# Kernel tuning notes

Hardware: AMD Instinct MI355X
Metric: run time of the kernel (lower is better)

The kernel has to match this reference:

```python
import jax, jax.numpy as jnp
import numpy as np
from jax import lax

D_MODEL = 200
N_LAYER = 12
NHEADS = 8
HEADDIM = 50
D_STATE = 64
D_INNER = 2 * D_MODEL            # 400
CONV_DIM = D_INNER + 2 * D_STATE  # 528 (ngroups=1)
D_IN_PROJ = 2 * D_INNER + 2 * D_STATE + NHEADS  # 936
D_CONV = 4
EPS = 1e-5


def rmsnorm(x, w):
    v = jnp.mean(jnp.square(x), axis=-1, keepdims=True)
    return x * lax.rsqrt(v + EPS) * w


def groupnorm(x, groups, g, b):
    B, C, H, W = x.shape
    xg = x.reshape(B, groups, C // groups, H, W)
    mu = jnp.mean(xg, axis=(2, 3, 4), keepdims=True)
    var = jnp.mean(jnp.square(xg - mu), axis=(2, 3, 4), keepdims=True)
    xn = ((xg - mu) * lax.rsqrt(var + EPS)).reshape(B, C, H, W)
    return xn * g[:, None, None] + b[:, None, None]


def patch_embed(x, pe_conv_w, proj_in_w, gn_g, gn_b, spec_w):
    b, c, l, d = x.shape
    # time path: 'b c l d' -> (b, 1, c*l, d), conv -> (b, 25, c*l, 8)
    time_x = x.reshape(b, 1, c * l, d)
    t = lax.conv_general_dilated(time_x, proj_in_w, (1, 25), ((0, 0), (24, 24)),
                                 dimension_numbers=('NCHW', 'OIHW', 'NCHW'))
    t = jax.nn.gelu(groupnorm(t, 5, gn_g, gn_b), approximate=False)
    time_emb = t.transpose(0, 2, 1, 3).reshape(b, c, l, D_MODEL)
    # freq path: rfft over patch dim, norm='forward'
    spec = jnp.abs(jnp.fft.rfft(x, axis=-1, norm='forward'))  # (b,c,l,101)
    spec_emb = jnp.einsum('bclf,df->bcld', spec, spec_w)
    patch = time_emb + spec_emb
    # depthwise 7x7 positional conv over (d, c, l)
    pos = lax.conv_general_dilated(patch.transpose(0, 3, 1, 2), pe_conv_w, (1, 1),
                                   ((3, 3), (3, 3)),
                                   dimension_numbers=('NCHW', 'OIHW', 'NCHW'),
                                   feature_group_count=D_MODEL)
    return patch + pos.transpose(0, 2, 3, 1)


def ssd_scan(xh, dt, B, C, A, D):
    # xh: (b,l,h,p)  dt: (b,l,h)  B,C: (b,l,n)  A,D: (h,)
    b, l, h, p = xh.shape

    def step(state, inp):
        x_t, dt_t, B_t, C_t = inp
        dA = jnp.exp(dt_t * A)  # (b,h)
        state = state * dA[:, :, None, None] + \
            (dt_t[:, :, None, None] * x_t[:, :, :, None]) * B_t[:, None, None, :]
        y = jnp.einsum('bhpn,bn->bhp', state, C_t)
        return state, y

    state0 = jnp.zeros((b, h, p, D_STATE), xh.dtype)
    _, ys = lax.scan(step, state0,
                     (xh.transpose(1, 0, 2, 3), dt.transpose(1, 0, 2),
                      B.transpose(1, 0, 2), C.transpose(1, 0, 2)))
    return ys.transpose(1, 0, 2, 3) + xh * D[None, None, :, None]


def mamba2(u, in_w, conv_w, conv_b, dt_bias, A_log, D, gn_w, out_w):
    b, l, _ = u.shape
    zxbcdt = u @ in_w.T  # (b,l,936)
    z = zxbcdt[..., :D_INNER]
    xBC = zxbcdt[..., D_INNER:D_INNER + CONV_DIM]
    dt = jax.nn.softplus(zxbcdt[..., D_INNER + CONV_DIM:] + dt_bias)  # (b,l,8)
    # causal depthwise conv1d, kernel 4
    xc = lax.conv_general_dilated(xBC.transpose(0, 2, 1), conv_w, (1,), ((D_CONV - 1, 0),),
                                  dimension_numbers=('NCH', 'OIH', 'NCH'),
                                  feature_group_count=CONV_DIM)
    xBC = jax.nn.silu((xc + conv_b[:, None]).transpose(0, 2, 1))
    x = xBC[..., :D_INNER].reshape(b, l, NHEADS, HEADDIM)
    Bm = xBC[..., D_INNER:D_INNER + D_STATE]
    Cm = xBC[..., D_INNER + D_STATE:]
    y = ssd_scan(x, dt, Bm, Cm, -jnp.exp(A_log), D).reshape(b, l, D_INNER)
    y = rmsnorm(y * jax.nn.silu(z), gn_w)  # RMSNormGated, norm_before_gate=False
    return y @ out_w.T


@jax.checkpoint
def layer(hidden, residual, norm_w, in_w, conv_w, conv_b, dt_bias, A_log, D, gn_w, out_w):
    residual = hidden + residual
    hidden = mamba2(rmsnorm(residual, norm_w), in_w, conv_w, conv_b, dt_bias, A_log, D, gn_w, out_w)
    return hidden, residual


def forward(x, pe_conv_w, proj_in_w, gn_g, gn_b, spec_w, norm_w, in_proj_w, conv_w, conv_b,
            dt_bias, A_log, D, gnorm_w, out_proj_w, norm_f_w, head_w, head_b):
    b, c, l, d = x.shape
    hidden = patch_embed(x, pe_conv_w, proj_in_w, gn_g, gn_b, spec_w).reshape(b, c * l, d)
    residual = jnp.zeros_like(hidden)
    for i in range(N_LAYER):
        hidden, residual = layer(hidden, residual, norm_w[i], in_proj_w[i], conv_w[i],
                                 conv_b[i], dt_bias[i], A_log[i], D[i], gnorm_w[i], out_proj_w[i])
    hidden = rmsnorm(hidden + residual, norm_f_w).reshape(b, c, l, d)
    return hidden @ head_w.T + head_b


def setup_inputs():
    key = jax.random.key(0)
    ks = jax.random.split(key, 12)
    B, CH, L, P = 16, 19, 30, 200

    def g(k, shape, scale):
        return jax.random.normal(k, shape, jnp.float32) * scale

    dt = jax.random.uniform(ks[8], (N_LAYER, NHEADS), jnp.float32, 1e-3, 0.1)
    return {
        'x': g(ks[0], (B, CH, L, P), 1.0),
        'pe_conv_w': g(ks[1], (D_MODEL, 1, 7, 7), 0.15),
        'proj_in_w': g(ks[2], (25, 1, 1, 49), 0.14),
        'gn_g': jnp.ones(25, jnp.float32),
        'gn_b': jnp.zeros(25, jnp.float32),
        'spec_w': g(ks[3], (D_MODEL, 101), 0.1),
        'norm_w': jnp.ones((N_LAYER, D_MODEL), jnp.float32),
        'in_proj_w': g(ks[4], (N_LAYER, D_IN_PROJ, D_MODEL), 0.07),
        'conv_w': g(ks[5], (N_LAYER, CONV_DIM, 1, D_CONV), 0.4),
        'conv_b': jnp.zeros((N_LAYER, CONV_DIM), jnp.float32),
        'dt_bias': jnp.log(jnp.expm1(dt)),
        'A_log': jnp.log(jax.random.uniform(ks[9], (N_LAYER, NHEADS), jnp.float32, 1.0, 16.0)),
        'D': jnp.ones((N_LAYER, NHEADS), jnp.float32),
        'gnorm_w': jnp.ones((N_LAYER, D_INNER), jnp.float32),
        'out_proj_w': g(ks[6], (N_LAYER, D_MODEL, D_INNER), 0.05),
        'norm_f_w': jnp.ones(D_MODEL, jnp.float32),
        'head_w': g(ks[7], (D_MODEL, D_MODEL), 0.07),
        'head_b': jnp.zeros(D_MODEL, jnp.float32),
    }


def reference(x, pe_conv_w, proj_in_w, gn_g, gn_b, spec_w, norm_w, in_proj_w, conv_w, conv_b,
              dt_bias, A_log, D, gnorm_w, out_proj_w, norm_f_w, head_w, head_b):
    return forward(x, pe_conv_w, proj_in_w, gn_g, gn_b, spec_w, norm_w, in_proj_w, conv_w,
                   conv_b, dt_bias, A_log, D, gnorm_w, out_proj_w, norm_f_w, head_w, head_b)
```

## Files before the change

kernel.cpp:

```cpp
#include <hip/hip_runtime.h>
#include <hip/hip_bf16.h>
#include <math.h>

#define D_MODEL   200
#define N_LAYER   12
#define NHEADS    8
#define HEADDIM   50
#define D_STATE   64
#define D_INNER   400
#define CONV_DIM  528
#define D_IN_PROJ 936
#define D_CONV    4
#define EPS       1e-5f

#define BATCH 16
#define CH    19
#define LLEN  30
#define SEQ   570
#define NTOK  9120
#define NFREQ 101

typedef __attribute__((ext_vector_type(8))) short s8v;
typedef __attribute__((ext_vector_type(4))) float f32x4;

__device__ __forceinline__ short f2bf(float f) {
    unsigned u = __float_as_uint(f);
    u += 0x7FFFu + ((u >> 16) & 1u);
    return (short)(u >> 16);
}

__global__ __launch_bounds__(256) void gemm_bf16(
    const short* __restrict__ A, const short* __restrict__ W,
    const float* __restrict__ bias, float* __restrict__ C,
    int M, int N, int Kp, int accum)
{
    __shared__ __align__(16) short As[128][40];
    __shared__ __align__(16) short Ws[128][40];

    int bm = blockIdx.y * 128;
    int bn = blockIdx.x * 128;
    int tid = threadIdx.x;
    int lane = tid & 63;
    int wv = tid >> 6;
    int wm = wv & 1, wn = wv >> 1;
    int lm = lane & 15, lg = lane >> 4;

    int sr = tid >> 1;
    int sh_ = (tid & 1) * 16;

    f32x4 acc[4][4];
#pragma unroll
    for (int i = 0; i < 4; i++)
#pragma unroll
        for (int j = 0; j < 4; j++) acc[i][j] = (f32x4)0.f;

    for (int k0 = 0; k0 < Kp; k0 += 32) {
        {
            s8v v0 = (s8v)0, v1 = (s8v)0;
            if (bm + sr < M) {
                const short* ga = A + (size_t)(bm + sr) * Kp + k0 + sh_;
                v0 = *(const s8v*)ga;
                v1 = *(const s8v*)(ga + 8);
            }
            *(s8v*)&As[sr][sh_] = v0;
            *(s8v*)&As[sr][sh_ + 8] = v1;
        }
        {
            s8v v0 = (s8v)0, v1 = (s8v)0;
            if (bn + sr < N) {
                const short* gw = W + (size_t)(bn + sr) * Kp + k0 + sh_;
                v0 = *(const s8v*)gw;
                v1 = *(const s8v*)(gw + 8);
            }
            *(s8v*)&Ws[sr][sh_] = v0;
            *(s8v*)&Ws[sr][sh_ + 8] = v1;
        }
        __syncthreads();

        s8v af[4], bf[4];
#pragma unroll
        for (int i = 0; i < 4; i++)
            af[i] = *(const s8v*)&As[wm * 64 + i * 16 + lm][lg * 8];
#pragma unroll
        for (int j = 0; j < 4; j++)
            bf[j] = *(const s8v*)&Ws[wn * 64 + j * 16 + lm][lg * 8];
#pragma unroll
        for (int i = 0; i < 4; i++)
#pragma unroll
            for (int j = 0; j < 4; j++)
                acc[i][j] = __builtin_amdgcn_mfma_f32_16x16x32_bf16(
                    af[i], bf[j], acc[i][j], 0, 0, 0);
        __syncthreads();
    }

#pragma unroll
    for (int j = 0; j < 4; j++) {
        int n = bn + wn * 64 + j * 16 + lm;
        if (n >= N) continue;
        float bv = bias ? bias[n] : 0.f;
#pragma unroll
        for (int i = 0; i < 4; i++) {
            int mbase = bm + wm * 64 + i * 16 + lg * 4;
#pragma unroll
            for (int r = 0; r < 4; r++) {
                int m = mbase + r;
                if (m >= M) continue;
                size_t idx = (size_t)m * N + n;
                float v = acc[i][j][r] + bv;
                if (accum) v += C[idx];
                C[idx] = v;
            }
        }
    }
}

__global__ __launch_bounds__(256) void gemm_nt(
    const float* __restrict__ A, const float* __restrict__ W,
    const float* __restrict__ bias, float* __restrict__ C,
    int M, int N, int K, int accum)
{
    const int BM = 128, BK = 16;
    __shared__ float As[16][BM + 4];
    __shared__ float Ws[16][BM + 4];

    int bm = blockIdx.y * BM;
    int bn = blockIdx.x * BM;
    int tid = threadIdx.x;
    int lr = tid >> 1;
    int lc = (tid & 1) * 8;
    int tx = tid & 15;
    int ty = tid >> 4;

    float acc[8][8];
#pragma unroll
    for (int i = 0; i < 8; i++)
#pragma unroll
        for (int j = 0; j < 8; j++) acc[i][j] = 0.f;

    for (int k0 = 0; k0 < K; k0 += BK) {
#pragma unroll
        for (int i = 0; i < 8; i++) {
            int gr = bm + lr, gk = k0 + lc + i;
            As[lc + i][lr] = (gr < M && gk < K) ? A[(size_t)gr * K + gk] : 0.f;
        }
#pragma unroll
        for (int i = 0; i < 8; i++) {
            int gr = bn + lr, gk = k0 + lc + i;
            Ws[lc + i][lr] = (gr < N && gk < K) ? W[(size_t)gr * K + gk] : 0.f;
        }
        __syncthreads();
#pragma unroll
        for (int kk = 0; kk < BK; kk++) {
            float a[8], bv[8];
#pragma unroll
            for (int i = 0; i < 8; i++) a[i] = As[kk][ty * 8 + i];
#pragma unroll
            for (int j = 0; j < 8; j++) bv[j] = Ws[kk][tx * 8 + j];
#pragma unroll
            for (int i = 0; i < 8; i++)
#pragma unroll
                for (int j = 0; j < 8; j++)
                    acc[i][j] = fmaf(a[i], bv[j], acc[i][j]);
        }
        __syncthreads();
    }

#pragma unroll
    for (int i = 0; i < 8; i++) {
        int gm = bm + ty * 8 + i;
        if (gm >= M) continue;
#pragma unroll
        for (int j = 0; j < 8; j++) {
            int gn = bn + tx * 8 + j;
            if (gn >= N) continue;
            float v = acc[i][j];
            if (bias) v += bias[gn];
            if (accum) v += C[(size_t)gm * N + gn];
            C[(size_t)gm * N + gn] = v;
        }
    }
}

// ... 158 lines not shown
#pragma unroll
    for (int k = 0; k < 49; k++) wreg[k] = wl[k * 16 + dd];

    for (int o = tid; o < 4 * 30 * 16; o += 256) {
        int r2 = o >> 4;
        int l = r2 % 30, ci = r2 / 30;
        int c = c0 + ci;
        if (c >= CH) continue;
        float acc = pl[((ci + 3) * 30 + l) * 16 + dd];
#pragma unroll
        for (int i = 0; i < 7; i++) {
#pragma unroll
            for (int j = 0; j < 7; j++) {
                int ll = l + j - 3;
                if (ll < 0 || ll >= LLEN) continue;
                acc = fmaf(pl[((ci + i) * 30 + ll) * 16 + dd], wreg[i * 7 + j], acc);
            }
        }
        if (d < 200) hidden[((size_t)(b * CH + c) * LLEN + l) * 200 + d] = acc;
    }
}

__global__ __launch_bounds__(64) void add_rmsnorm_kernel(
    const float* __restrict__ hidden, float* __restrict__ residual,
    const float* __restrict__ wn, float* __restrict__ u,
    short* __restrict__ ubf, int first)
{
    int m = blockIdx.x;
    int lane = threadIdx.x;
    const float* hr = hidden + (size_t)m * 200;
    float* rr = residual + (size_t)m * 200;
    float v[4];
    float ss = 0.f;
#pragma unroll
    for (int i = 0; i < 4; i++) {
        int k = lane + i * 64;
        float xv = 0.f;
        if (k < 200) {
            xv = hr[k] + (first ? 0.f : rr[k]);
            rr[k] = xv;
        }
        v[i] = xv;
        ss = fmaf(xv, xv, ss);
    }
#pragma unroll
    for (int o = 32; o; o >>= 1) ss += __shfl_xor(ss, o, 64);
    float rstd = rsqrtf(ss * (1.f / 200.f) + EPS);
#pragma unroll
    for (int i = 0; i < 4; i++) {
        int k = lane + i * 64;
        float val = v[i] * rstd * ((k < 200) ? wn[k] : 0.f);
        if (k < 200 && u) u[(size_t)m * 200 + k] = val;
        if (ubf) {
            if (k < 200) ubf[(size_t)m * 224 + k] = f2bf(val);
            else if (k < 224) ubf[(size_t)m * 224 + k] = 0;
        }
    }
}

__global__ __launch_bounds__(256) void norm_dt_kernel(
    const float* __restrict__ hidden, float* __restrict__ residual,
    const float* __restrict__ wn, short* __restrict__ ubf,
    const float* __restrict__ Win, const float* __restrict__ dt_bias,
    float* __restrict__ dtb, int layer, int first)
{
    int m = blockIdx.x;
    int tid = threadIdx.x;
    __shared__ float su[200];
    __shared__ float rs[4];
    float xv = 0.f;
    if (tid < 200) {
        xv = hidden[(size_t)m * 200 + tid] + (first ? 0.f : residual[(size_t)m * 200 + tid]);
        residual[(size_t)m * 200 + tid] = xv;
    }
    float ss = xv * xv;
#pragma unroll
    for (int o = 32; o; o >>= 1) ss += __shfl_xor(ss, o, 64);
    int lane = tid & 63, w = tid >> 6;
    if (lane == 0) rs[w] = ss;
    __syncthreads();
    float rstd = rsqrtf((rs[0] + rs[1] + rs[2] + rs[3]) * (1.f / 200.f) + EPS);
    if (tid < 200) {
        float val = xv * rstd * wn[tid];
        su[tid] = val;
        ubf[(size_t)m * 224 + tid] = f2bf(val);
    } else if (tid < 224) {
        ubf[(size_t)m * 224 + tid] = 0;
    }
    __syncthreads();
    int h = tid >> 5, l = tid & 31;
    const float* wr = Win + (size_t)layer * D_IN_PROJ * 200 + (size_t)(928 + h) * 200;
    float s = 0.f;
    for (int k = l; k < 200; k += 32) s = fmaf(su[k], wr[k], s);
    s += __shfl_xor(s, 16, 32);
    s += __shfl_xor(s, 8, 32);
    s += __shfl_xor(s, 4, 32);
    s += __shfl_xor(s, 2, 32);
    s += __shfl_xor(s, 1, 32);
    if (l == 0) {
        float raw = s + dt_bias[layer * NHEADS + h];
        dtb[(size_t)m * NHEADS + h] = (raw > 20.f) ? raw : log1pf(expf(raw));
    }
}

__global__ __launch_bounds__(256) void dt_gemv_kernel(
    const float* __restrict__ u, const float* __restrict__ Win,
    const float* __restrict__ dt_bias, float* __restrict__ dtb, int layer)
{
    int tid = threadIdx.x;
    int tok = blockIdx.x * 4 + (tid >> 6);
    int head = (tid >> 3) & 7;
    int l8 = tid & 7;
    const float* ur = u + (size_t)tok * 200;
    const float* wr = Win + (size_t)layer * D_IN_PROJ * 200 + (size_t)(928 + head) * 200;
    float s = 0.f;
    for (int k = l8; k < 200; k += 8) s = fmaf(ur[k], wr[k], s);
    s += __shfl_xor(s, 1, 64);
    s += __shfl_xor(s, 2, 64);
    s += __shfl_xor(s, 4, 64);
    if (l8 == 0) {
        float raw = s + dt_bias[layer * NHEADS + head];
        dtb[(size_t)tok * NHEADS + head] = (raw > 20.f) ? raw : log1pf(expf(raw));
    }
}

__global__ __launch_bounds__(256) void dtconv2_kernel(
    const float* __restrict__ zxbcdt, const float* __restrict__ cw,
    const float* __restrict__ cb, float* __restrict__ xBC, int layer)
{
    int b = blockIdx.x, tt = blockIdx.y;
    int t0 = tt * 8;
    __shared__ float zs[11][528];
    const float* cwl = cw + (size_t)layer * CONV_DIM * 4;
    const float* cbl = cb + (size_t)layer * CONV_DIM;
    for (int i = threadIdx.x; i < 11 * 528; i += 256) {
        int r = i / 528, ch = i - r * 528;
        int t = t0 - 3 + r;
        zs[r][ch] = (t >= 0 && t < SEQ)
                        ? zxbcdt[(size_t)(b * SEQ + t) * D_IN_PROJ + D_INNER + ch] : 0.f;
    }
    __syncthreads();
    for (int o = threadIdx.x; o < 8 * 528; o += 256) {
        int tr = o / 528, ch = o - tr * 528;
        int t = t0 + tr;
        if (t >= SEQ) continue;
        float acc = cbl[ch];
#pragma unroll
        for (int k = 0; k < 4; k++)
            acc = fmaf(zs[tr + k][ch], cwl[ch * 4 + k], acc);
        xBC[(size_t)(b * SEQ + t) * CONV_DIM + ch] = acc / (1.f + expf(-acc));
    }
}

__global__ __launch_bounds__(512) void ssd_scanA_kernel(
    const float* __restrict__ xBC, const float* __restrict__ dtb,
    const float* __restrict__ A_log, const float* __restrict__ Dv,
    float* __restrict__ ylocal, float* __restrict__ Pref,
    float* __restrict__ Sbuf, float* __restrict__ Pd,
    int layer, int lchunk, int nchunk)
{
    int b = blockIdx.x, c = blockIdx.y;
    int tid = threadIdx.x;
    int h = tid >> 6, p = tid & 63;
    float A = -expf(A_log[layer * NHEADS + h]);
    float Dh = Dv[layer * NHEADS + h];

    __shared__ __align__(16) float sh[3][2][536];
    int t0 = c * lchunk;
    int npairs = lchunk >> 1;

    for (int j = 0; j < 2 && j < npairs; j++) {
        if (tid < 264) {
            int wch = (tid >= 132) ? 1 : 0;
            int fidx = tid - wch * 132;
            int tq = t0 + 2 * j + wch;
            float4 v = ((const float4*)(xBC + (size_t)(b * SEQ + tq) * CONV_DIM))[fidx];
            *(float4*)&sh[j][wch][fidx * 4] = v;
        } else if (tid < 280) {
            int e = tid - 264, tok = e >> 3, hd = e & 7;
            sh[j][tok][528 + hd] = dtb[(size_t)(b * SEQ + t0 + 2 * j + tok) * NHEADS + hd];
        }
    }
    __syncthreads();

    float s[64];
#pragma unroll
    for (int n = 0; n < 64; n++) s[n] = 0.f;
    float pacc = 1.f;

    for (int i = 0; i < npairs; i++) {
        int t = t0 + 2 * i;
        int buf = i % 3;
        int nb = (i + 2) % 3;
        bool pf = (i + 2 < npairs);
        float4 rx;
        float rdt = 0.f;
        int wch = 0, fidx = 0;
        if (pf) {
            if (tid < 264) {
                wch = (tid >= 132) ? 1 : 0;
                fidx = tid - wch * 132;
                int tq = t + 4 + wch;
                rx = ((const float4*)(xBC + (size_t)(b * SEQ + tq) * CONV_DIM))[fidx];
            } else if (tid < 280) {
                int e = tid - 264, tok = e >> 3, hd = e & 7;
                rdt = dtb[(size_t)(b * SEQ + t + 4 + tok) * NHEADS + hd];
            }
        }
#pragma unroll
        for (int k = 0; k < 2; k++) {
            float dtv = sh[buf][k][528 + h];
            float xp  = (p < HEADDIM) ? sh[buf][k][h * HEADDIM + p] : 0.f;
            float dA = __expf(dtv * A);
            float u  = dtv * xp;
            pacc *= dA;
            const float4* B4 = (const float4*)&sh[buf][k][D_INNER];
            const float4* C4 = (const float4*)&sh[buf][k][D_INNER + D_STATE];
            float y0 = 0.f, y1 = 0.f, y2 = 0.f, y3 = 0.f;
#pragma unroll
            for (int n4 = 0; n4 < 16; n4++) {
                float4 bq = B4[n4];
                float4 cq = C4[n4];
                float t0v = fmaf(s[4 * n4 + 0], dA, u * bq.x);
                float t1v = fmaf(s[4 * n4 + 1], dA, u * bq.y);
                float t2v = fmaf(s[4 * n4 + 2], dA, u * bq.z);
                float t3v = fmaf(s[4 * n4 + 3], dA, u * bq.w);
                s[4 * n4 + 0] = t0v; s[4 * n4 + 1] = t1v;
                s[4 * n4 + 2] = t2v; s[4 * n4 + 3] = t3v;
                y0 = fmaf(t0v, cq.x, y0);
                y1 = fmaf(t1v, cq.y, y1);
                y2 = fmaf(t2v, cq.z, y2);
                y3 = fmaf(t3v, cq.w, y3);
            }
            if (p < HEADDIM)
                ylocal[(size_t)(b * SEQ + t + k) * D_INNER + h * HEADDIM + p] =
                    fmaf(xp, Dh, (y0 + y1) + (y2 + y3));
            if (p == 0)
                Pref[(size_t)(b * SEQ + t + k) * NHEADS + h] = pacc;
        }
        if (pf) {
            if (tid < 264) *(float4*)&sh[nb][wch][fidx * 4] = rx;
            else if (tid < 280) { int e = tid - 264; sh[nb][e >> 3][528 + (e & 7)] = rdt; }
        }
        __syncthreads();
    }

    if (p < HEADDIM) {
        float* Sb = Sbuf + ((size_t)((b * NHEADS + h) * nchunk + c)) * (HEADDIM * 64)
                    + p * 64;
#pragma unroll
        for (int n4 = 0; n4 < 16; n4++)
            ((float4*)Sb)[n4] = make_float4(s[4 * n4], s[4 * n4 + 1],
                                            s[4 * n4 + 2], s[4 * n4 + 3]);
    }
    if (p == 0) Pd[(b * NHEADS + h) * nchunk + c] = pacc;
}

__global__ __launch_bounds__(512) void ssd_state_kernel(
    const float* __restrict__ xBC, const float* __restrict__ dtb,
    const float* __restrict__ A_log, float* __restrict__ Sbuf,
    float* __restrict__ Pd, int layer, int lchunk, int nchunk)
{
    int b = blockIdx.x, c = blockIdx.y;
    int tid = threadIdx.x;
    int h = tid >> 6, p = tid & 63;
    float A = -expf(A_log[layer * NHEADS + h]);

    __shared__ float sh[2][544];
    int t0 = c * lchunk, tend = t0 + lchunk;

    {
        const float* base = xBC + (size_t)(b * SEQ + t0) * CONV_DIM;
        sh[0][tid] = base[tid];
        if (tid < 24) {
            int e2 = 512 + tid;
            sh[0][e2] = (e2 < 528) ? base[e2]
                                   : dtb[(size_t)(b * SEQ + t0) * NHEADS + (e2 - 528)];
        }
    }
    __syncthreads();

    float s[64];
#pragma unroll
    for (int n = 0; n < 64; n++) s[n] = 0.f;
    float pacc = 1.f;

    for (int t = t0; t < tend; t++) {
        int cur = (t - t0) & 1, nxt = cur ^ 1;
        float pf0 = 0.f, pf1 = 0.f;
        if (t + 1 < tend) {
            const float* base = xBC + (size_t)(b * SEQ + t + 1) * CONV_DIM;
            pf0 = base[tid];
            if (tid < 24) {
                int e2 = 512 + tid;
                pf1 = (e2 < 528) ? base[e2]
                                 : dtb[(size_t)(b * SEQ + t + 1) * NHEADS + (e2 - 528)];
            }
        }
        float dtv = sh[cur][528 + h];
        float xp  = (p < HEADDIM) ? sh[cur][h * HEADDIM + p] : 0.f;
        float dA = __expf(dtv * A);
        float u  = dtv * xp;
        pacc *= dA;
        const float4* B4 = (const float4*)&sh[cur][D_INNER];
#pragma unroll
        for (int n4 = 0; n4 < 16; n4++) {
            float4 bq = B4[n4];
            s[4 * n4 + 0] = fmaf(s[4 * n4 + 0], dA, u * bq.x);
            s[4 * n4 + 1] = fmaf(s[4 * n4 + 1], dA, u * bq.y);
            s[4 * n4 + 2] = fmaf(s[4 * n4 + 2], dA, u * bq.z);
            s[4 * n4 + 3] = fmaf(s[4 * n4 + 3], dA, u * bq.w);
        }
        if (t + 1 < tend) {
            sh[nxt][tid] = pf0;
            if (tid < 24) sh[nxt][512 + tid] = pf1;
        }
        __syncthreads();
    }

    if (p < HEADDIM) {
        float* Sb = Sbuf + ((size_t)((b * NHEADS + h) * nchunk + c)) * (HEADDIM * 64)
                    + p * 64;
#pragma unroll
        for (int n4 = 0; n4 < 16; n4++)
            ((float4*)Sb)[n4] = make_float4(s[4 * n4], s[4 * n4 + 1],
                                            s[4 * n4 + 2], s[4 * n4 + 3]);
    }
    if (p == 0) Pd[(b * NHEADS + h) * nchunk + c] = pacc;
}

__global__ __launch_bounds__(256) void ssd_scan2b_kernel(
    float* __restrict__ Sbuf, const float* __restrict__ Pd, int nchunk)
{
    int bh = blockIdx.x;
    int e = blockIdx.y * 256 + threadIdx.x;
    if (e >= HEADDIM * 64) return;
    float* base = Sbuf + (size_t)bh * nchunk * (HEADDIM * 64) + e;
    const float* pd = Pd + bh * nchunk;
    float cur = 0.f;
    for (int c = 0; c < nchunk; c++) {
        float l = base[(size_t)c * (HEADDIM * 64)];
        base[(size_t)c * (HEADDIM * 64)] = cur;
        cur = fmaf(pd[c], cur, l);
    }
}

__global__ __launch_bounds__(512) void ssd_corr_kernel(
    const float* __restrict__ xBC, const float* __restrict__ zxbcdt,
    const float* __restrict__ ylocal, const float* __restrict__ Pref,
    const float* __restrict__ Sbuf, const float* __restrict__ gw,
    short* __restrict__ ybf, int layer, int lchunk, int nchunk)
{
    int b = blockIdx.x, c = blockIdx.y;
    int tid = threadIdx.x;
    int h = tid >> 6, p = tid & 63;
    float gval = (p < HEADDIM) ? gw[(size_t)layer * D_INNER + h * HEADDIM + p] : 0.f;

    __shared__ __align__(16) float Cst[2][2][64];
    __shared__ float pfs[2][2][8];
    __shared__ float red[2][2][8];
    int t0 = c * lchunk;
    int npairs = lchunk >> 1;

    float s0[64];
    if (p < HEADDIM) {
        const float* Sb = Sbuf + ((size_t)((b * NHEADS + h) * nchunk + c)) * (HEADDIM * 64)
                          + p * 64;
#pragma unroll
        for (int n4 = 0; n4 < 16; n4++) {
            float4 v = ((const float4*)Sb)[n4];
            s0[4 * n4] = v.x; s0[4 * n4 + 1] = v.y;
            s0[4 * n4 + 2] = v.z; s0[4 * n4 + 3] = v.w;
        }
    } else {
#pragma unroll
        for (int n = 0; n < 64; n++) s0[n] = 0.f;
    }

    int col = h * HEADDIM + ((p < HEADDIM) ? p : 0);

    if (tid < 128) {
        int k = tid >> 6, n = tid & 63;
        Cst[0][k][n] = xBC[(size_t)(b * SEQ + t0 + k) * CONV_DIM + D_INNER + D_STATE + n];
    } else if (tid < 144) {
        int e = tid - 128, k = e >> 3, hd = e & 7;
        pfs[0][k][hd] = Pref[(size_t)(b * SEQ + t0 + k) * NHEADS + hd];
    }
    float ylr[2], zvr[2];
#pragma unroll
    for (int k = 0; k < 2; k++) {
        ylr[k] = ylocal[(size_t)(b * SEQ + t0 + k) * D_INNER + col];
        zvr[k] = zxbcdt[(size_t)(b * SEQ + t0 + k) * D_IN_PROJ + col];
    }
    __syncthreads();

    for (int i = 0; i < npairs; i++) {
        int t = t0 + 2 * i;
        int buf = i & 1, nb = buf ^ 1;
        bool pf = (i + 1 < npairs);
        float rc = 0.f, rpf = 0.f, yln[2], zvn[2];
        if (pf) {
            if (tid < 128) {
                int k = tid >> 6, n = tid & 63;
                rc = xBC[(size_t)(b * SEQ + t + 2 + k) * CONV_DIM + D_INNER + D_STATE + n];
            } else if (tid < 144) {
                int e = tid - 128, k = e >> 3, hd = e & 7;
                rpf = Pref[(size_t)(b * SEQ + t + 2 + k) * NHEADS + hd];
            }
#pragma unroll
            for (int k = 0; k < 2; k++) {
                yln[k] = ylocal[(size_t)(b * SEQ + t + 2 + k) * D_INNER + col];
                zvn[k] = zxbcdt[(size_t)(b * SEQ + t + 2 + k) * D_IN_PROJ + col];
            }
        }
        float g0 = 0.f, g1 = 0.f;
#pragma unroll
        for (int k = 0; k < 2; k++) {
            const float4* C4 = (const float4*)&Cst[buf][k][0];
            float c0 = 0.f, c1 = 0.f, c2 = 0.f, c3 = 0.f;
#pragma unroll
            for (int n4 = 0; n4 < 16; n4++) {
                float4 cq = C4[n4];
                c0 = fmaf(s0[4 * n4 + 0], cq.x, c0);
                c1 = fmaf(s0[4 * n4 + 1], cq.y, c1);
                c2 = fmaf(s0[4 * n4 + 2], cq.z, c2);
                c3 = fmaf(s0[4 * n4 + 3], cq.w, c3);
            }
            float corr = (c0 + c1) + (c2 + c3);
            float yv = fmaf(pfs[buf][k][h], corr, ylr[k]);
            float zv = zvr[k];
            float gg = yv * (zv / (1.f + expf(-zv)));
            gg = (p < HEADDIM) ? gg : 0.f;
            if (k == 0) g0 = gg; else g1 = gg;
        }
        float gs0 = g0 * g0, gs1 = g1 * g1;
#pragma unroll
        for (int o = 32; o; o >>= 1) {
            gs0 += __shfl_xor(gs0, o, 64);
            gs1 += __shfl_xor(gs1, o, 64);
        }
        if (p == 0) { red[buf][0][h] = gs0; red[buf][1][h] = gs1; }
        if (pf) {
            if (tid < 128) { int k = tid >> 6, n = tid & 63; Cst[nb][k][n] = rc; }
            else if (tid < 144) { int e = tid - 128; pfs[nb][e >> 3][e & 7] = rpf; }
            ylr[0] = yln[0]; ylr[1] = yln[1];
            zvr[0] = zvn[0]; zvr[1] = zvn[1];
        }
        __syncthreads();
        float tot0 = (red[buf][0][0] + red[buf][0][1]) + (red[buf][0][2] + red[buf][0][3]) +
                     (red[buf][0][4] + red[buf][0][5]) + (red[buf][0][6] + red[buf][0][7]);
        float tot1 = (red[buf][1][0] + red[buf][1][1]) + (red[buf][1][2] + red[buf][1][3]) +
                     (red[buf][1][4] + red[buf][1][5]) + (red[buf][1][6] + red[buf][1][7]);
        float rstd0 = rsqrtf(tot0 * (1.f / D_INNER) + EPS);
        float rstd1 = rsqrtf(tot1 * (1.f / D_INNER) + EPS);
        size_t row0 = (size_t)(b * SEQ + t) * 416;
        size_t row1 = (size_t)(b * SEQ + t + 1) * 416;
        if (p < HEADDIM) {
            ybf[row0 + h * HEADDIM + p] = f2bf(g0 * rstd0 * gval);
            ybf[row1 + h * HEADDIM + p] = f2bf(g1 * rstd1 * gval);
        } else {
            int widx = h * 14 + (p - HEADDIM);
            if (widx < 16) {
                ybf[row0 + 400 + widx] = 0;
                ybf[row1 + 400 + widx] = 0;
            }
        }
    }
}

__global__ __launch_bounds__(512) void ssd_out_kernel(
    const float* __restrict__ xBC, const float* __restrict__ dtb,
    const float* __restrict__ A_log, const float* __restrict__ Dv,
    const float* __restrict__ Sbuf, float* __restrict__ y,
    int layer, int lchunk, int nchunk)
{
    int b = blockIdx.x, c = blockIdx.y;
    int tid = threadIdx.x;
    int h = tid >> 6, p = tid & 63;
    float A = -expf(A_log[layer * NHEADS + h]);
    float Dh = Dv[layer * NHEADS + h];

    __shared__ float sh[2][544];
    int t0 = c * lchunk, tend = t0 + lchunk;

    {
        const float* base = xBC + (size_t)(b * SEQ + t0) * CONV_DIM;
        sh[0][tid] = base[tid];
        if (tid < 24) {
            int e2 = 512 + tid;
            sh[0][e2] = (e2 < 528) ? base[e2]
                                   : dtb[(size_t)(b * SEQ + t0) * NHEADS + (e2 - 528)];
        }
    }

    float s[64];
    if (p < HEADDIM) {
        const float* Sb = Sbuf + ((size_t)((b * NHEADS + h) * nchunk + c)) * (HEADDIM * 64)
                          + p * 64;
#pragma unroll
        for (int n4 = 0; n4 < 16; n4++) {
            float4 v = ((const float4*)Sb)[n4];
            s[4 * n4] = v.x; s[4 * n4 + 1] = v.y; s[4 * n4 + 2] = v.z; s[4 * n4 + 3] = v.w;
        }
    } else {
#pragma unroll
        for (int n = 0; n < 64; n++) s[n] = 0.f;
    }
    __syncthreads();

    for (int t = t0; t < tend; t++) {
        int cur = (t - t0) & 1, nxt = cur ^ 1;
        float pf0 = 0.f, pf1 = 0.f;
        if (t + 1 < tend) {
            const float* base = xBC + (size_t)(b * SEQ + t + 1) * CONV_DIM;
            pf0 = base[tid];
            if (tid < 24) {
                int e2 = 512 + tid;
                pf1 = (e2 < 528) ? base[e2]
                                 : dtb[(size_t)(b * SEQ + t + 1) * NHEADS + (e2 - 528)];
            }
        }
        float dtv = sh[cur][528 + h];
        float xp  = (p < HEADDIM) ? sh[cur][h * HEADDIM + p] : 0.f;
        float dA = __expf(dtv * A);
        float u  = dtv * xp;
        const float4* B4 = (const float4*)&sh[cur][D_INNER];
        const float4* C4 = (const float4*)&sh[cur][D_INNER + D_STATE];
        float y0 = 0.f, y1 = 0.f, y2 = 0.f, y3 = 0.f;
#pragma unroll
        for (int n4 = 0; n4 < 16; n4++) {
            float4 bq = B4[n4];
            float4 cq = C4[n4];
            float t0v = fmaf(s[4 * n4 + 0], dA, u * bq.x);
            float t1v = fmaf(s[4 * n4 + 1], dA, u * bq.y);
            float t2v = fmaf(s[4 * n4 + 2], dA, u * bq.z);
            float t3v = fmaf(s[4 * n4 + 3], dA, u * bq.w);
            s[4 * n4 + 0] = t0v; s[4 * n4 + 1] = t1v;
            s[4 * n4 + 2] = t2v; s[4 * n4 + 3] = t3v;
            y0 = fmaf(t0v, cq.x, y0);
            y1 = fmaf(t1v, cq.y, y1);
            y2 = fmaf(t2v, cq.z, y2);
            y3 = fmaf(t3v, cq.w, y3);
        }
        if (p < HEADDIM) {
            float yv = (y0 + y1) + (y2 + y3);
            y[(size_t)(b * SEQ + t) * D_INNER + h * HEADDIM + p] = fmaf(xp, Dh, yv);
        }
        if (t + 1 < tend) {
            sh[nxt][tid] = pf0;
            if (tid < 24) sh[nxt][512 + tid] = pf1;
        }
        __syncthreads();
    }
}

__global__ __launch_bounds__(256) void gate_norm_kernel(
    float* __restrict__ y, const float* __restrict__ zxbcdt,
    const float* __restrict__ gw, short* __restrict__ ybf, int layer)
{
    int m = blockIdx.x;
    __shared__ float buf[D_INNER];
    __shared__ float red[4];
    const float* z = zxbcdt + (size_t)m * D_IN_PROJ;
    float* yr = y + (size_t)m * D_INNER;
    const float* gwl = gw + (size_t)layer * D_INNER;
    float ss = 0.f;
    for (int k = threadIdx.x; k < D_INNER; k += 256) {
        float zv = z[k];
        float sz = zv / (1.f + expf(-zv));
        float g = yr[k] * sz;
        buf[k] = g;
        ss = fmaf(g, g, ss);
    }
    int lane = threadIdx.x & 63, w = threadIdx.x >> 6;
#pragma unroll
    for (int o = 32; o; o >>= 1) ss += __shfl_xor(ss, o, 64);
    if (lane == 0) red[w] = ss;
    __syncthreads();
    float tot = red[0] + red[1] + red[2] + red[3];
    float rstd = rsqrtf(tot * (1.f / D_INNER) + EPS);
    for (int k = threadIdx.x; k < 416; k += 256) {
        if (k < D_INNER) {
            float v = buf[k] * rstd * gwl[k];
            yr[k] = v;
            if (ybf) ybf[(size_t)m * 416 + k] = f2bf(v);
        } else if (ybf) {
            ybf[(size_t)m * 416 + k] = 0;
        }
    }
}

extern "C" void kernel_launch(void* const* d_in, const int* in_sizes, int n_in,
                              void* d_out, int out_size, void* d_ws, size_t ws_size,
                              hipStream_t stream)
{
    const float* x         = (const float*)d_in[0];
    const float* pe_conv_w = (const float*)d_in[1];
    const float* proj_in_w = (const float*)d_in[2];
    const float* gn_g      = (const float*)d_in[3];
    const float* gn_b      = (const float*)d_in[4];
    const float* spec_w    = (const float*)d_in[5];
    const float* norm_w    = (const float*)d_in[6];
    const float* in_proj_w = (const float*)d_in[7];
    const float* conv_w    = (const float*)d_in[8];
    const float* conv_b    = (const float*)d_in[9];
    const float* dt_bias   = (const float*)d_in[10];
    const float* A_log     = (const float*)d_in[11];
    const float* Dv        = (const float*)d_in[12];
    const float* gnorm_w   = (const float*)d_in[13];
    const float* out_proj_w= (const float*)d_in[14];
    const float* norm_f_w  = (const float*)d_in[15];
    const float* head_w    = (const float*)d_in[16];
    const float* head_b    = (const float*)d_in[17];
    float* out = (float*)d_out;
    float* ws  = (float*)d_ws;

    const size_t needA = 31650304ull * sizeof(float);
    int fast = (ws_size >= needA) ? 1 : 0;

    int nchunk, lchunk;
    float *residual = ws, *hidden = ws + 1824000;
    float *zxbcdt, *xBC, *dtb, *Sbuf, *Pd;
    float *ubuf = nullptr, *ybuf = nullptr, *ybuf_s = nullptr, *Pref = nullptr;
    short *w_in_bf = nullptr, *w_out_bf = nullptr, *w_head_bf = nullptr,
          *w_spec_bf = nullptr, *csmat_bf = nullptr, *x_bf = nullptr,
          *ubuf_bf = nullptr, *ybuf_bf = nullptr, *magb_bf = nullptr;

    if (fast) {
        nchunk = 15; lchunk = 38;
        zxbcdt = ws + 3648000;
        xBC    = ws + 12184320;
        dtb    = ws + 16999680;
        Sbuf   = ws + 17072640;
        Pd     = ws + 23216640;
        short* pool = (short*)(ws + 23218560);
        w_in_bf   = pool;
        w_out_bf  = pool + 2515968;
        w_head_bf = pool + 3514368;
        w_spec_bf = pool + 3559168;
        ubuf_bf   = pool + 3584768;
        ybuf_bf   = pool + 5627648;
        ybuf_s    = ws + 27929344;
        Pref      = ws + 31577344;
        csmat_bf  = (short*)(Sbuf + 4000000);
        x_bf      = (short*)(Sbuf + 4100000);
        magb_bf   = (short*)(Sbuf + 5200000);
    } else {
        nchunk = 6; lchunk = 95;
        ubuf   = ws + 3648000;
        zxbcdt = ws + 5472000;
        xBC    = ws + 14008320;
        dtb    = ws + 18823680;
        ybuf   = ws + 18896640;
        Sbuf   = ws + 1824000;
        Pd     = ws + 5470000;
    }

    float* traw  = fast ? Sbuf : ybuf;
    float* patch = zxbcdt;
    float* csout = fast ? (Sbuf + 2000000) : (xBC + 50000);
    float* csmat = xBC;
    float* magb  = fast ? nullptr : (xBC + 2000000);
    float* stats = dtb;

    if (fast) {
        cast_pad_kernel<<<(12 * 936 * 224 + 255) / 256, 256, 0, stream>>>(
            in_proj_w, w_in_bf, 12 * 936, 200, 224);
        cast_pad_kernel<<<(12 * 200 * 416 + 255) / 256, 256, 0, stream>>>(
            out_proj_w, w_out_bf, 12 * 200, 400, 416);
        cast_pad_kernel<<<(200 * 224 + 255) / 256, 256, 0, stream>>>(
            head_w, w_head_bf, 200, 200, 224);
        cast_pad_kernel<<<(200 * 128 + 255) / 256, 256, 0, stream>>>(
            spec_w, w_spec_bf, 200, 101, 128);
        cast_pad_kernel<<<(9120 * 224 + 255) / 256, 256, 0, stream>>>(
            x, x_bf, 9120, 200, 224);
        dft_init_bf_kernel<<<(202 * 224 + 255) / 256, 256, 0, stream>>>(csmat_bf);
    } else {
        dft_init_kernel<<<(202 * 200 + 255) / 256, 256, 0, stream>>>(csmat);
    }

    time_conv_kernel<<<NTOK, 256, 0, stream>>>(x, proj_in_w, traw);
    gn_stats_kernel<<<80, 256, 0, stream>>>(traw, stats);
    gn_gelu_kernel<<<(NTOK * 200 + 255) / 256, 256, 0, stream>>>(traw, stats, gn_g, gn_b, patch);
    if (fast) {
        gemm_bf16<<<dim3(2, 72), 256, 0, stream>>>(x_bf, csmat_bf, nullptr, csout,
                                                   NTOK, 202, 224, 0);
        mag_bf_kernel<<<(NTOK * 128 + 255) / 256, 256, 0, stream>>>(csout, magb_bf);
        gemm_bf16<<<dim3(2, 72), 256, 0, stream>>>(magb_bf, w_spec_bf, nullptr, patch,
                                                   NTOK, 200, 128, 1);
    } else {
        gemm_nt<<<dim3(2, 72), 256, 0, stream>>>(x, csmat, nullptr, csout, NTOK, 202, 200, 0);
        mag_kernel<<<(NTOK * NFREQ + 255) / 256, 256, 0, stream>>>(csout, magb);
        gemm_nt<<<dim3(2, 72), 256, 0, stream>>>(magb, spec_w, nullptr, patch,
                                                 NTOK, 200, NFREQ, 1);
    }
    pe_conv3_kernel<<<dim3(16, 13, 5), 256, 0, stream>>>(patch, pe_conv_w, hidden);

    for (int i = 0; i < N_LAYER; i++) {
        if (fast) {
            norm_dt_kernel<<<NTOK, 256, 0, stream>>>(hidden, residual, norm_w + i * 200,
                                                     ubuf_bf, in_proj_w, dt_bias, dtb,
                                                     i, (i == 0) ? 1 : 0);
            gemm_bf16<<<dim3(8, 72), 256, 0, stream>>>(
                ubuf_bf, w_in_bf + (size_t)i * 936 * 224, nullptr, zxbcdt,
                NTOK, D_IN_PROJ, 224, 0);
        } else {
            add_rmsnorm_kernel<<<NTOK, 64, 0, stream>>>(hidden, residual, norm_w + i * 200,
                                                        ubuf, nullptr, (i == 0) ? 1 : 0);
            dt_gemv_kernel<<<NTOK / 4, 256, 0, stream>>>(ubuf, in_proj_w, dt_bias, dtb, i);
            gemm_nt<<<dim3(8, 72), 256, 0, stream>>>(
                ubuf, in_proj_w + (size_t)i * D_IN_PROJ * 200, nullptr, zxbcdt,
                NTOK, D_IN_PROJ, 200, 0);
        }
        dtconv2_kernel<<<dim3(16, 72), 256, 0, stream>>>(zxbcdt, conv_w, conv_b, xBC, i);
        {
            dim3 g(BATCH, nchunk);
            if (fast) {
                ssd_scanA_kernel<<<g, 512, 0, stream>>>(xBC, dtb, A_log, Dv,
                                                        ybuf_s, Pref, Sbuf, Pd,
                                                        i, lchunk, nchunk);
                ssd_scan2b_kernel<<<dim3(BATCH * NHEADS, 13), 256, 0, stream>>>(Sbuf, Pd, nchunk);
                ssd_corr_kernel<<<g, 512, 0, stream>>>(
                    xBC, zxbcdt, ybuf_s, Pref, Sbuf, gnorm_w, ybuf_bf, i, lchunk, nchunk);
                gemm_bf16<<<dim3(2, 72), 256, 0, stream>>>(
                    ybuf_bf, w_out_bf + (size_t)i * 200 * 416, nullptr, hidden,
                    NTOK, 200, 416, 0);
            } else {
                ssd_state_kernel<<<g, 512, 0, stream>>>(xBC, dtb, A_log, Sbuf, Pd,
                                                        i, lchunk, nchunk);
                ssd_scan2b_kernel<<<dim3(BATCH * NHEADS, 13), 256, 0, stream>>>(Sbuf, Pd, nchunk);
                ssd_out_kernel<<<g, 512, 0, stream>>>(xBC, dtb, A_log, Dv, Sbuf, ybuf,
                                                      i, lchunk, nchunk);
                gate_norm_kernel<<<NTOK, 256, 0, stream>>>(ybuf, zxbcdt, gnorm_w, nullptr, i);
                gemm_nt<<<dim3(2, 72), 256, 0, stream>>>(
                    ybuf, out_proj_w + (size_t)i * 200 * D_INNER, nullptr, hidden,
                    NTOK, 200, D_INNER, 0);
            }
        }
    }

    add_rmsnorm_kernel<<<NTOK, 64, 0, stream>>>(hidden, residual, norm_f_w,
                                                fast ? nullptr : ubuf,
                                                fast ? ubuf_bf : nullptr, 0);
    if (fast) {
        gemm_bf16<<<dim3(2, 72), 256, 0, stream>>>(ubuf_bf, w_head_bf, head_b, out,
                                                   NTOK, 200, 224, 0);
    } else {
        gemm_nt<<<dim3(2, 72), 256, 0, stream>>>(ubuf, head_w, head_b, out,
                                                 NTOK, 200, 200, 0);
    }
}
```

Baseline: 2.565 ms.

## Restructure chunked SSD scan into state-only pass plus fused output rescan with bf16 B/C

Replaces the scanA pass, which produced local outputs, prefix decays and chunk states, and the correction pass with two kernels. The first pass now computes only the chunk-final states. The second pass rescans each chunk from the carried-in state, computing the output, gate and norm directly. This drops the ylocal and Pref intermediate buffers and their global traffic, and shrinks the workspace. It costs recomputing the recurrence twice. B and C are staged in shared memory as bf16, which lowers LDS footprint and bandwidth but loses precision in the state update.

```diff
diff --git a/kernel.cpp b/kernel.cpp
--- a/kernel.cpp
+++ b/kernel.cpp
@@ -28,6 +28,13 @@
     u += 0x7FFFu + ((u >> 16) & 1u);
     return (short)(u >> 16);
 }
+__device__ __forceinline__ uint2 packbf4(float4 v) {
+    unsigned a = (unsigned short)f2bf(v.x), b = (unsigned short)f2bf(v.y);
+    unsigned c = (unsigned short)f2bf(v.z), d = (unsigned short)f2bf(v.w);
+    return make_uint2(a | (b << 16), c | (d << 16));
+}
+__device__ __forceinline__ float bflo(unsigned d) { return __uint_as_float(d << 16); }
+__device__ __forceinline__ float bfhi(unsigned d) { return __uint_as_float(d & 0xffff0000u); }
 
 __global__ __launch_bounds__(256) void gemm_bf16(
     const short* __restrict__ A, const short* __restrict__ W,
@@ -492,33 +499,35 @@
     }
 }
 
-__global__ __launch_bounds__(512) void ssd_scanA_kernel(
+__global__ __launch_bounds__(512) void ssd_state4_kernel(
     const float* __restrict__ xBC, const float* __restrict__ dtb,
-    const float* __restrict__ A_log, const float* __restrict__ Dv,
-    float* __restrict__ ylocal, float* __restrict__ Pref,
-    float* __restrict__ Sbuf, float* __restrict__ Pd,
-    int layer, int lchunk, int nchunk)
+    const float* __restrict__ A_log, float* __restrict__ Sbuf,
+    float* __restrict__ Pd, int layer, int lchunk, int nchunk)
 {
     int b = blockIdx.x, c = blockIdx.y;
     int tid = threadIdx.x;
     int h = tid >> 6, p = tid & 63;
     float A = -expf(A_log[layer * NHEADS + h]);
-    float Dh = Dv[layer * NHEADS + h];
-
-    __shared__ __align__(16) float sh[3][2][536];
+
+    __shared__ __align__(16) float shx[2][2][400];
+    __shared__ __align__(16) uint2 shB[2][2][16];
+    __shared__ float shdt[2][2][8];
     int t0 = c * lchunk;
     int npairs = lchunk >> 1;
 
-    for (int j = 0; j < 2 && j < npairs; j++) {
-        if (tid < 264) {
-            int wch = (tid >= 132) ? 1 : 0;
-            int fidx = tid - wch * 132;
-            int tq = t0 + 2 * j + wch;
-            float4 v = ((const float4*)(xBC + (size_t)(b * SEQ + tq) * CONV_DIM))[fidx];
-            *(float4*)&sh[j][wch][fidx * 4] = v;
-        } else if (tid < 280) {
-            int e = tid - 264, tok = e >> 3, hd = e & 7;
-            sh[j][tok][528 + hd] = dtb[(size_t)(b * SEQ + t0 + 2 * j + tok) * NHEADS + hd];
+    {
+        if (tid < 200) {
+            int tok = (tid >= 100) ? 1 : 0;
+            int fidx = tid - tok * 100;
+            float4 v = ((const float4*)(xBC + (size_t)(b * SEQ + t0 + tok) * CONV_DIM))[fidx];
+            *(float4*)&shx[0][tok][fidx * 4] = v;
+        } else if (tid < 232) {
+            int e = tid - 200, tok = e >> 4, q = e & 15;
+            float4 v = ((const float4*)(xBC + (size_t)(b * SEQ + t0 + tok) * CONV_DIM))[100 + q];
+            shB[0][tok][q] = packbf4(v);
+        } else if (tid < 248) {
+            int e = tid - 232, tok = e >> 3, hd = e & 7;
+            shdt[0][tok][hd] = dtb[(size_t)(b * SEQ + t0 + tok) * NHEADS + hd];
         }
     }
     __syncthreads();
@@ -530,57 +539,52 @@
 
     for (int i = 0; i < npairs; i++) {
         int t = t0 + 2 * i;
-        int buf = i % 3;
-        int nb = (i + 2) % 3;
-        bool pf = (i + 2 < npairs);
-        float4 rx;
-        float rdt = 0.f;
-        int wch = 0, fidx = 0;
+        int buf = i & 1, nb = buf ^ 1;
+        bool pf = (2 * i + 2 < lchunk);
+        float4 rx; float rdt = 0.f;
+        int tokr = 0, fidxr = 0, qB = -1;
         if (pf) {
-            if (tid < 264) {
-                wch = (tid >= 132) ? 1 : 0;
-                fidx = tid - wch * 132;
-                int tq = t + 4 + wch;
-                rx = ((const float4*)(xBC + (size_t)(b * SEQ + tq) * CONV_DIM))[fidx];
-            } else if (tid < 280) {
-                int e = tid - 264, tok = e >> 3, hd = e & 7;
-                rdt = dtb[(size_t)(b * SEQ + t + 4 + tok) * NHEADS + hd];
+            if (tid < 200) {
+                tokr = (tid >= 100) ? 1 : 0;
+                fidxr = tid - tokr * 100;
+                rx = ((const float4*)(xBC + (size_t)(b * SEQ + t + 2 + tokr) * CONV_DIM))[fidxr];
+            } else if (tid < 232) {
+                int e = tid - 200; tokr = e >> 4; qB = e & 15;
+                rx = ((const float4*)(xBC + (size_t)(b * SEQ + t + 2 + tokr) * CONV_DIM))[100 + qB];
+            } else if (tid < 248) {
+                int e = tid - 232; tokr = e >> 3; int hd = e & 7;
+                rdt = dtb[(size_t)(b * SEQ + t + 2 + tokr) * NHEADS + hd];
             }
         }
 #pragma unroll
         for (int k = 0; k < 2; k++) {
-            float dtv = sh[buf][k][528 + h];
-            float xp  = (p < HEADDIM) ? sh[buf][k][h * HEADDIM + p] : 0.f;
+            float dtv = shdt[buf][k][h];
+            float xp  = (p < HEADDIM) ? shx[buf][k][h * HEADDIM + p] : 0.f;
             float dA = __expf(dtv * A);
             float u  = dtv * xp;
             pacc *= dA;
-            const float4* B4 = (const float4*)&sh[buf][k][D_INNER];
-            const float4* C4 = (const float4*)&sh[buf][k][D_INNER + D_STATE];
-            float y0 = 0.f, y1 = 0.f, y2 = 0.f, y3 = 0.f;
-#pragma unroll
-            for (int n4 = 0; n4 < 16; n4++) {
-                float4 bq = B4[n4];
-                float4 cq = C4[n4];
-                float t0v = fmaf(s[4 * n4 + 0], dA, u * bq.x);
-                float t1v = fmaf(s[4 * n4 + 1], dA, u * bq.y);
-                float t2v = fmaf(s[4 * n4 + 2], dA, u * bq.z);
-                float t3v = fmaf(s[4 * n4 + 3], dA, u * bq.w);
-                s[4 * n4 + 0] = t0v; s[4 * n4 + 1] = t1v;
-                s[4 * n4 + 2] = t2v; s[4 * n4 + 3] = t3v;
-                y0 = fmaf(t0v, cq.x, y0);
-                y1 = fmaf(t1v, cq.y, y1);
-                y2 = fmaf(t2v, cq.z, y2);
-                y3 = fmaf(t3v, cq.w, y3);
-            }
-            if (p < HEADDIM)
-                ylocal[(size_t)(b * SEQ + t + k) * D_INNER + h * HEADDIM + p] =
-                    fmaf(xp, Dh, (y0 + y1) + (y2 + y3));
-            if (p == 0)
-                Pref[(size_t)(b * SEQ + t + k) * NHEADS + h] = pacc;
+            const uint4* Bp = (const uint4*)&shB[buf][k][0];
+#pragma unroll
+            for (int r = 0; r < 8; r++) {
+                uint4 w = Bp[r];
+                float b0 = bflo(w.x), b1 = bfhi(w.x);
+                float b2 = bflo(w.y), b3 = bfhi(w.y);
+                float b4 = bflo(w.z), b5 = bfhi(w.z);
+                float b6 = bflo(w.w), b7 = bfhi(w.w);
+                s[8 * r + 0] = fmaf(s[8 * r + 0], dA, u * b0);
+                s[8 * r + 1] = fmaf(s[8 * r + 1], dA, u * b1);
+                s[8 * r + 2] = fmaf(s[8 * r + 2], dA, u * b2);
+                s[8 * r + 3] = fmaf(s[8 * r + 3], dA, u * b3);
+                s[8 * r + 4] = fmaf(s[8 * r + 4], dA, u * b4);
+                s[8 * r + 5] = fmaf(s[8 * r + 5], dA, u * b5);
+                s[8 * r + 6] = fmaf(s[8 * r + 6], dA, u * b6);
+                s[8 * r + 7] = fmaf(s[8 * r + 7], dA, u * b7);
+            }
         }
         if (pf) {
-            if (tid < 264) *(float4*)&sh[nb][wch][fidx * 4] = rx;
-            else if (tid < 280) { int e = tid - 264; sh[nb][e >> 3][528 + (e & 7)] = rdt; }
+            if (tid < 200) *(float4*)&shx[nb][tokr][fidxr * 4] = rx;
+            else if (tid < 232) shB[nb][tokr][qB] = packbf4(rx);
+            else if (tid < 248) { int e = tid - 232; shdt[nb][e >> 3][e & 7] = rdt; }
         }
         __syncthreads();
     }
@@ -685,93 +689,129 @@
     }
 }
 
-__global__ __launch_bounds__(512) void ssd_corr_kernel(
-    const float* __restrict__ xBC, const float* __restrict__ zxbcdt,
-    const float* __restrict__ ylocal, const float* __restrict__ Pref,
-    const float* __restrict__ Sbuf, const float* __restrict__ gw,
-    short* __restrict__ ybf, int layer, int lchunk, int nchunk)
+__global__ __launch_bounds__(512) void ssd_out_fused4_kernel(
+    const float* __restrict__ xBC, const float* __restrict__ dtb,
+    const float* __restrict__ zxbcdt, const float* __restrict__ A_log,
+    const float* __restrict__ Dv, const float* __restrict__ Sbuf,
+    const float* __restrict__ gw, short* __restrict__ ybf,
+    int layer, int lchunk, int nchunk)
 {
     int b = blockIdx.x, c = blockIdx.y;
     int tid = threadIdx.x;
     int h = tid >> 6, p = tid & 63;
+    float A = -expf(A_log[layer * NHEADS + h]);
+    float Dh = Dv[layer * NHEADS + h];
     float gval = (p < HEADDIM) ? gw[(size_t)layer * D_INNER + h * HEADDIM + p] : 0.f;
 
-    __shared__ __align__(16) float Cst[2][2][64];
-    __shared__ float pfs[2][2][8];
+    __shared__ __align__(16) float shx[2][2][400];
+    __shared__ __align__(16) uint2 shBC[2][2][32];
+    __shared__ float shdt[2][2][8];
+    __shared__ __align__(16) float shz[2][2][400];
     __shared__ float red[2][2][8];
     int t0 = c * lchunk;
     int npairs = lchunk >> 1;
 
-    float s0[64];
+    {
+        if (tid < 200) {
+            int tok = (tid >= 100) ? 1 : 0;
+            int fidx = tid - tok * 100;
+            float4 v = ((const float4*)(xBC + (size_t)(b * SEQ + t0 + tok) * CONV_DIM))[fidx];
+            *(float4*)&shx[0][tok][fidx * 4] = v;
+        } else if (tid < 264) {
+            int e = tid - 200, tok = e >> 5, q = e & 31;
+            float4 v = ((const float4*)(xBC + (size_t)(b * SEQ + t0 + tok) * CONV_DIM))[100 + q];
+            shBC[0][tok][q] = packbf4(v);
+        } else if (tid < 280) {
+            int e = tid - 264, tok = e >> 3, hd = e & 7;
+            shdt[0][tok][hd] = dtb[(size_t)(b * SEQ + t0 + tok) * NHEADS + hd];
+        } else if (tid < 480) {
+            int e = tid - 280;
+            int tok = (e >= 100) ? 1 : 0;
+            int fidx = e - tok * 100;
+            float4 v = ((const float4*)(zxbcdt + (size_t)(b * SEQ + t0 + tok) * D_IN_PROJ))[fidx];
+            *(float4*)&shz[0][tok][fidx * 4] = v;
+        }
+    }
+
+    float s[64];
     if (p < HEADDIM) {
         const float* Sb = Sbuf + ((size_t)((b * NHEADS + h) * nchunk + c)) * (HEADDIM * 64)
                           + p * 64;
 #pragma unroll
         for (int n4 = 0; n4 < 16; n4++) {
             float4 v = ((const float4*)Sb)[n4];
-            s0[4 * n4] = v.x; s0[4 * n4 + 1] = v.y;
-            s0[4 * n4 + 2] = v.z; s0[4 * n4 + 3] = v.w;
+            s[4 * n4] = v.x; s[4 * n4 + 1] = v.y; s[4 * n4 + 2] = v.z; s[4 * n4 + 3] = v.w;
         }
     } else {
 #pragma unroll
-        for (int n = 0; n < 64; n++) s0[n] = 0.f;
-    }
-
-    int col = h * HEADDIM + ((p < HEADDIM) ? p : 0);
-
-    if (tid < 128) {
-        int k = tid >> 6, n = tid & 63;
-        Cst[0][k][n] = xBC[(size_t)(b * SEQ + t0 + k) * CONV_DIM + D_INNER + D_STATE + n];
-    } else if (tid < 144) {
-        int e = tid - 128, k = e >> 3, hd = e & 7;
-        pfs[0][k][hd] = Pref[(size_t)(b * SEQ + t0 + k) * NHEADS + hd];
-    }
-    float ylr[2], zvr[2];
-#pragma unroll
-    for (int k = 0; k < 2; k++) {
-        ylr[k] = ylocal[(size_t)(b * SEQ + t0 + k) * D_INNER + col];
-        zvr[k] = zxbcdt[(size_t)(b * SEQ + t0 + k) * D_IN_PROJ + col];
+        for (int n = 0; n < 64; n++) s[n] = 0.f;
     }
     __syncthreads();
 
     for (int i = 0; i < npairs; i++) {
         int t = t0 + 2 * i;
         int buf = i & 1, nb = buf ^ 1;
-        bool pf = (i + 1 < npairs);
-        float rc = 0.f, rpf = 0.f, yln[2], zvn[2];
+        bool pf = (2 * i + 2 < lchunk);
+        float4 rx, rz; float rdt = 0.f;
+        int tokr = 0, fidxr = 0, qBC = -1, ztokr = 0, zfidxr = 0;
         if (pf) {
-            if (tid < 128) {
-                int k = tid >> 6, n = tid & 63;
-                rc = xBC[(size_t)(b * SEQ + t + 2 + k) * CONV_DIM + D_INNER + D_STATE + n];
-            } else if (tid < 144) {
-                int e = tid - 128, k = e >> 3, hd = e & 7;
-                rpf = Pref[(size_t)(b * SEQ + t + 2 + k) * NHEADS + hd];
-            }
-#pragma unroll
-            for (int k = 0; k < 2; k++) {
-                yln[k] = ylocal[(size_t)(b * SEQ + t + 2 + k) * D_INNER + col];
-                zvn[k] = zxbcdt[(size_t)(b * SEQ + t + 2 + k) * D_IN_PROJ + col];
+            if (tid < 200) {
+                tokr = (tid >= 100) ? 1 : 0;
+                fidxr = tid - tokr * 100;
+                rx = ((const float4*)(xBC + (size_t)(b * SEQ + t + 2 + tokr) * CONV_DIM))[fidxr];
+            } else if (tid < 264) {
+                int e = tid - 200; tokr = e >> 5; qBC = e & 31;
+                rx = ((const float4*)(xBC + (size_t)(b * SEQ + t + 2 + tokr) * CONV_DIM))[100 + qBC];
+            } else if (tid < 280) {
+                int e = tid - 264; tokr = e >> 3; int hd = e & 7;
+                rdt = dtb[(size_t)(b * SEQ + t + 2 + tokr) * NHEADS + hd];
+            } else if (tid < 480) {
+                int e = tid - 280;
+                ztokr = (e >= 100) ? 1 : 0;
+                zfidxr = e - ztokr * 100;
+                rz = ((const float4*)(zxbcdt + (size_t)(b * SEQ + t + 2 + ztokr) * D_IN_PROJ))[zfidxr];
             }
         }
         float g0 = 0.f, g1 = 0.f;
 #pragma unroll
         for (int k = 0; k < 2; k++) {
-            const float4* C4 = (const float4*)&Cst[buf][k][0];
-            float c0 = 0.f, c1 = 0.f, c2 = 0.f, c3 = 0.f;
-#pragma unroll
-            for (int n4 = 0; n4 < 16; n4++) {
-                float4 cq = C4[n4];
-                c0 = fmaf(s0[4 * n4 + 0], cq.x, c0);
-                c1 = fmaf(s0[4 * n4 + 1], cq.y, c1);
-                c2 = fmaf(s0[4 * n4 + 2], cq.z, c2);
-                c3 = fmaf(s0[4 * n4 + 3], cq.w, c3);
-            }
-            float corr = (c0 + c1) + (c2 + c3);
-            float yv = fmaf(pfs[buf][k][h], corr, ylr[k]);
-            float zv = zvr[k];
-            float gg = yv * (zv / (1.f + expf(-zv)));
-            gg = (p < HEADDIM) ? gg : 0.f;
-            if (k == 0) g0 = gg; else g1 = gg;
+            float dtv = shdt[buf][k][h];
+            float xp  = (p < HEADDIM) ? shx[buf][k][h * HEADDIM + p] : 0.f;
+            float dA = __expf(dtv * A);
+            float u  = dtv * xp;
+            const uint4* Wp = (const uint4*)&shBC[buf][k][0];
+            float y0 = 0.f, y1 = 0.f, y2 = 0.f, y3 = 0.f;
+#pragma unroll
+            for (int r = 0; r < 8; r++) {
+                uint4 wB = Wp[r];
+                uint4 wC = Wp[8 + r];
+                float b0 = bflo(wB.x), b1 = bfhi(wB.x), b2 = bflo(wB.y), b3 = bfhi(wB.y);
+                float b4 = bflo(wB.z), b5 = bfhi(wB.z), b6 = bflo(wB.w), b7 = bfhi(wB.w);
+                float c0 = bflo(wC.x), c1 = bfhi(wC.x), c2 = bflo(wC.y), c3 = bfhi(wC.y);
+                float c4 = bflo(wC.z), c5 = bfhi(wC.z), c6 = bflo(wC.w), c7 = bfhi(wC.w);
+                float t0v = fmaf(s[8 * r + 0], dA, u * b0);
+                float t1v = fmaf(s[8 * r + 1], dA, u * b1);
+                float t2v = fmaf(s[8 * r + 2], dA, u * b2);
+                float t3v = fmaf(s[8 * r + 3], dA, u * b3);
+                float t4v = fmaf(s[8 * r + 4], dA, u * b4);
+                float t5v = fmaf(s[8 * r + 5], dA, u * b5);
+                float t6v = fmaf(s[8 * r + 6], dA, u * b6);
+                float t7v = fmaf(s[8 * r + 7], dA, u * b7);
+                s[8 * r + 0] = t0v; s[8 * r + 1] = t1v;
+                s[8 * r + 2] = t2v; s[8 * r + 3] = t3v;
+                s[8 * r + 4] = t4v; s[8 * r + 5] = t5v;
+                s[8 * r + 6] = t6v; s[8 * r + 7] = t7v;
+                y0 = fmaf(t0v, c0, y0); y1 = fmaf(t1v, c1, y1);
+                y2 = fmaf(t2v, c2, y2); y3 = fmaf(t3v, c3, y3);
+                y0 = fmaf(t4v, c4, y0); y1 = fmaf(t5v, c5, y1);
+                y2 = fmaf(t6v, c6, y2); y3 = fmaf(t7v, c7, y3);
+            }
+            if (p < HEADDIM) {
+                float yv = fmaf(xp, Dh, (y0 + y1) + (y2 + y3));
+                float zv = shz[buf][k][h * HEADDIM + p];
+                float gg = yv * (zv / (1.f + expf(-zv)));
+                if (k == 0) g0 = gg; else g1 = gg;
+            }
         }
         float gs0 = g0 * g0, gs1 = g1 * g1;
 #pragma unroll
@@ -781,10 +821,10 @@
         }
         if (p == 0) { red[buf][0][h] = gs0; red[buf][1][h] = gs1; }
         if (pf) {
-            if (tid < 128) { int k = tid >> 6, n = tid & 63; Cst[nb][k][n] = rc; }
-            else if (tid < 144) { int e = tid - 128; pfs[nb][e >> 3][e & 7] = rpf; }
-            ylr[0] = yln[0]; ylr[1] = yln[1];
-            zvr[0] = zvn[0]; zvr[1] = zvn[1];
+            if (tid < 200) *(float4*)&shx[nb][tokr][fidxr * 4] = rx;
+            else if (tid < 264) shBC[nb][tokr][qBC] = packbf4(rx);
+            else if (tid < 280) { int e = tid - 264; shdt[nb][e >> 3][e & 7] = rdt; }
+            else if (tid < 480) *(float4*)&shz[nb][ztokr][zfidxr * 4] = rz;
         }
         __syncthreads();
         float tot0 = (red[buf][0][0] + red[buf][0][1]) + (red[buf][0][2] + red[buf][0][3]) +
@@ -955,13 +995,13 @@
     float* out = (float*)d_out;
     float* ws  = (float*)d_ws;
 
-    const size_t needA = 31650304ull * sizeof(float);
+    const size_t needA = 27929344ull * sizeof(float);
     int fast = (ws_size >= needA) ? 1 : 0;
 
     int nchunk, lchunk;
     float *residual = ws, *hidden = ws + 1824000;
     float *zxbcdt, *xBC, *dtb, *Sbuf, *Pd;
-    float *ubuf = nullptr, *ybuf = nullptr, *ybuf_s = nullptr, *Pref = nullptr;
+    float *ubuf = nullptr, *ybuf = nullptr;
     short *w_in_bf = nullptr, *w_out_bf = nullptr, *w_head_bf = nullptr,
           *w_spec_bf = nullptr, *csmat_bf = nullptr, *x_bf = nullptr,
           *ubuf_bf = nullptr, *ybuf_bf = nullptr, *magb_bf = nullptr;
@@ -980,8 +1020,6 @@
         w_spec_bf = pool + 3559168;
         ubuf_bf   = pool + 3584768;
         ybuf_bf   = pool + 5627648;
-        ybuf_s    = ws + 27929344;
-        Pref      = ws + 31577344;
         csmat_bf  = (short*)(Sbuf + 4000000);
         x_bf      = (short*)(Sbuf + 4100000);
         magb_bf   = (short*)(Sbuf + 5200000);
@@ -1056,12 +1094,11 @@
         {
             dim3 g(BATCH, nchunk);
             if (fast) {
-                ssd_scanA_kernel<<<g, 512, 0, stream>>>(xBC, dtb, A_log, Dv,
-                                                        ybuf_s, Pref, Sbuf, Pd,
-                                                        i, lchunk, nchunk);
+                ssd_state4_kernel<<<g, 512, 0, stream>>>(xBC, dtb, A_log, Sbuf, Pd,
+                                                         i, lchunk, nchunk);
                 ssd_scan2b_kernel<<<dim3(BATCH * NHEADS, 13), 256, 0, stream>>>(Sbuf, Pd, nchunk);
-                ssd_corr_kernel<<<g, 512, 0, stream>>>(
-                    xBC, zxbcdt, ybuf_s, Pref, Sbuf, gnorm_w, ybuf_bf, i, lchunk, nchunk);
+                ssd_out_fused4_kernel<<<g, 512, 0, stream>>>(
+                    xBC, dtb, zxbcdt, A_log, Dv, Sbuf, gnorm_w, ybuf_bf, i, lchunk, nchunk);
                 gemm_bf16<<<dim3(2, 72), 256, 0, stream>>>(
                     ybuf_bf, w_out_bf + (size_t)i * 200 * 416, nullptr, hidden,
                     NTOK, 200, 416, 0);
```

New measurement: 2.597 ms. About the same (+1.3%).
